# Optimization experiments

Hardware: AMD Instinct MI355X
Metric: run time of the kernel (lower is better)

## Reference

```python
import jax, jax.numpy as jnp
import numpy as np

V, E, F, K, Y = 50000, 128, 256, 3, 1000  # vocab, embed, filters, kernel, labels


def setup_inputs() -> dict:
    key = jax.random.key(0)
    ks = jax.random.split(key, 8)
    x = jax.random.randint(ks[0], (16, 4096), 0, V)
    target = jax.random.randint(ks[1], (16,), 0, Y)
    embed_w = jax.random.normal(ks[2], (V, E), dtype=jnp.float32) * 0.02
    embed_w = embed_w.at[0].set(0.0)  # padding_idx=0
    conv_w = jax.random.normal(ks[3], (F, E, K), dtype=jnp.float32) * (1.0 / np.sqrt(E * K))
    conv_b = jnp.zeros((F,), dtype=jnp.float32)
    U_w = jax.random.normal(ks[4], (Y, F), dtype=jnp.float32) * (1.0 / np.sqrt(F))
    fc_w = jax.random.normal(ks[5], (Y, F), dtype=jnp.float32) * (1.0 / np.sqrt(F))
    fc_b = jnp.zeros((Y,), dtype=jnp.float32)
    return {"x": x, "target": target, "embed_w": embed_w, "conv_w": conv_w,
            "conv_b": conv_b, "U_w": U_w, "fc_w": fc_w, "fc_b": fc_b}


def reference(x, target, embed_w, conv_w, conv_b, U_w, fc_w, fc_b):
    # embedding lookup: (B, L, E); dropout is identity in eval mode
    h = embed_w[x]
    h = jnp.transpose(h, (0, 2, 1))  # (B, E, L)
    # conv1d, SAME padding (pad = floor(K/2) = 1 for K=3)
    h = jax.lax.conv_general_dilated(
        h, conv_w, window_strides=(1,), padding="SAME",
        dimension_numbers=("NCH", "OIH", "NCH"))
    h = jax.nn.relu(h + conv_b[None, :, None])  # (B, F, L)
    # label-wise attention: scores (B, Y, L), softmax over L
    scores = jnp.einsum("yf,bfl->byl", U_w, h)
    alpha = jax.nn.softmax(scores, axis=2)
    # attend: m (B, Y, F)
    m = jnp.einsum("byl,bfl->byf", alpha, h)
    # per-label dot with fc rows + bias -> logits (B, Y)
    logit = jnp.sum(fc_w[None] * m, axis=2) + fc_b
    # cross-entropy loss (target='drg')
    logp = jax.nn.log_softmax(logit, axis=1)
    loss = -jnp.mean(jnp.take_along_axis(logp, target[:, None], axis=1))
    return (logit, loss)
```

## Files before the change

kernel.cpp:

```cpp
#include <hip/hip_runtime.h>
#include <math.h>

using short8   = __attribute__((ext_vector_type(8)))  short;
using floatx4  = __attribute__((ext_vector_type(4)))  float;
using floatx16 = __attribute__((ext_vector_type(16))) float;
using uintx4   = __attribute__((ext_vector_type(4)))  unsigned int;

#define AS1 __attribute__((address_space(1)))
#define AS3 __attribute__((address_space(3)))

__device__ __forceinline__ unsigned short f2bf(float f) {
  union { float f; unsigned int u; } v; v.f = f;
  unsigned int r = v.u + 0x7FFFu + ((v.u >> 16) & 1u);
  return (unsigned short)(r >> 16);
}
__device__ __forceinline__ void gload_lds16(const void* g, void* l) {
  __builtin_amdgcn_global_load_lds((const AS1 unsigned int*)g, (AS3 unsigned int*)l, 16, 0, 0);
}

#define B_  16
#define L_  4096
#define E_  128
#define F_  256
#define Y_  1000

#define OFF_HLF   0u
#define OFF_UBF   33554432u
#define OFF_FBF   34078720u
#define OFF_WBF   34603008u
#define OFF_PART  34799616u
#define OFF_LOSST 35323904u

__global__ __launch_bounds__(256) void k_repack_u(const float* __restrict__ src,
                                                  unsigned short* __restrict__ dst) {
  int i = blockIdx.x * 256 + threadIdx.x;
  int y = i >> 8, f = i & 255;
  float v = (y < Y_) ? src[y * F_ + f] : 0.f;
  dst[i] = f2bf(v);
}

__global__ __launch_bounds__(256) void k_repack_w(const float* __restrict__ cw,
                                                  unsigned short* __restrict__ wbf) {
  int i = blockIdx.x * 256 + threadIdx.x;
  const float* s = cw + (size_t)i * 3;
  wbf[0 * 32768 + i] = f2bf(s[0]);
  wbf[1 * 32768 + i] = f2bf(s[1]);
  wbf[2 * 32768 + i] = f2bf(s[2]);
}

#define ET_STR 272
__global__ __launch_bounds__(256, 4) void k_conv(const unsigned short* __restrict__ wbf,
                                                 const float* __restrict__ conv_b,
                                                 const int* __restrict__ x,
                                                 const float* __restrict__ ew,
                                                 unsigned short* __restrict__ hlf) {
  __shared__ unsigned char et[66 * ET_STR];
  const int tid = threadIdx.x, bid = blockIdx.x;
  const int b = bid >> 6, l0 = (bid & 63) << 6;
  const int w = tid >> 6, lane = tid & 63, c = lane & 15, q = lane >> 4;
  const int* xb = x + b * L_;
  for (int s = tid; s < 1056; s += 256) {
    int row = s >> 4, sg = s & 15;
    int l = l0 - 1 + row;
    int idx = (l >= 0 && l < L_) ? xb[l] : 0;
    const float4* src = (const float4*)(ew + (size_t)idx * E_ + sg * 8);
    float4 a = src[0], bb = src[1];
    uintx4 v;
    v.x = (unsigned int)f2bf(a.x) | ((unsigned int)f2bf(a.y) << 16);
    v.y = (unsigned int)f2bf(a.z) | ((unsigned int)f2bf(a.w) << 16);
    v.z = (unsigned int)f2bf(bb.x) | ((unsigned int)f2bf(bb.y) << 16);
    v.w = (unsigned int)f2bf(bb.z) | ((unsigned int)f2bf(bb.w) << 16);
    *(uintx4*)(et + row * ET_STR + sg * 16) = v;
  }
  __syncthreads();
  const int fw = w * 64;
  floatx4 acc[4][4];
  #pragma unroll
  for (int ms = 0; ms < 4; ++ms)
    #pragma unroll
    for (int nt = 0; nt < 4; ++nt) acc[ms][nt] = (floatx4){0.f, 0.f, 0.f, 0.f};
  #pragma unroll
  for (int d = 0; d < 3; ++d)
    #pragma unroll
    for (int kq = 0; kq < 4; ++kq) {
      short8 aa[4], bb[4];
      #pragma unroll
      for (int ms = 0; ms < 4; ++ms)
        aa[ms] = *(const short8*)(et + (ms * 16 + q * 4 + (0) + c * 0 + 0 + (ms * 0)) * 0 +
                                  (ms * 16 + c + d) * ET_STR + kq * 64 + q * 16);
      #pragma unroll
      for (int nt = 0; nt < 4; ++nt)
        bb[nt] = *(const short8*)((const unsigned char*)wbf +
                   ((size_t)(d * F_ + fw + nt * 16 + c) * E_ + kq * 32 + q * 8) * 2);
      #pragma unroll
      for (int ms = 0; ms < 4; ++ms)
        #pragma unroll
        for (int nt = 0; nt < 4; ++nt)
          acc[ms][nt] = __builtin_amdgcn_mfma_f32_16x16x32_bf16(aa[ms], bb[nt], acc[ms][nt], 0, 0, 0);
    }
  #pragma unroll
  for (int nt = 0; nt < 4; ++nt) {
    int f = fw + nt * 16 + c;
    float bias = conv_b[f];
    #pragma unroll
    for (int ms = 0; ms < 4; ++ms)
      #pragma unroll
      for (int r = 0; r < 4; ++r) {
        int l = l0 + ms * 16 + q * 4 + r;
        float v = acc[ms][nt][r] + bias;
        v = v > 0.f ? v : 0.f;
        hlf[((size_t)b * L_ + l) * F_ + f] = f2bf(v);
      }
  }
}

__global__ __launch_bounds__(256, 2) void k_attn(const unsigned short* __restrict__ ubf,
                                                 const unsigned short* __restrict__ fbf,
                                                 const unsigned short* __restrict__ hlf,
                                                 float2* __restrict__ part) {
  __shared__ unsigned char lds[32768];
  const int tid = threadIdx.x;
  const int w = tid >> 6, lane = tid & 63, lo = lane & 31, hi = lane >> 5;
  const int bid = blockIdx.x;
  const int xcd = bid & 7, r0 = bid >> 3;
  const int b = xcd * 2 + (r0 & 1);
  const int r2 = r0 >> 1, yt = r2 & 7, chunk = r2 >> 3;
  const int y0 = yt << 7, yw = y0 + w * 32;
  short8 uf[16], ff[16];
  #pragma unroll
  for (int ks = 0; ks < 16; ++ks) {
    size_t off = ((size_t)(yw + lo) * F_ + ks * 16 + hi * 8) * 2;
    uf[ks] = *(const short8*)((const unsigned char*)ubf + off);
    ff[ks] = *(const short8*)((const unsigned char*)fbf + off);
  }
  float num[16], den[16];
  #pragma unroll
  for (int r = 0; r < 16; ++r) { num[r] = 0.f; den[r] = 0.f; }
  const unsigned char* hlfb = (const unsigned char*)hlf + (size_t)b * L_ * (F_ * 2);
  const int l0base = chunk << 10;

#define STAGE(dstbuf, l0v)                                                      \
  {                                                                             \
    unsigned char* dstb = (dstbuf);                                             \
    _Pragma("unroll")                                                           \
    for (int ii = 0; ii < 4; ++ii) {                                            \
      int i = w * 4 + ii;                                                       \
      int r = 2 * i + hi;                                                       \
      int g = lo ^ r;                                                           \
      gload_lds16(hlfb + (size_t)((l0v) + r) * 512 + g * 16, dstb + i * 1024);  \
    }                                                                           \
  }

  STAGE(lds, l0base);
  __syncthreads();
  for (int it = 0; it < 32; ++it) {
    unsigned char* cur = lds + ((it & 1) << 14);
    if (it < 31) STAGE(lds + (((it & 1) ^ 1) << 14), l0base + (it + 1) * 32);
    floatx16 S = {0.f,0.f,0.f,0.f,0.f,0.f,0.f,0.f,0.f,0.f,0.f,0.f,0.f,0.f,0.f,0.f};
    floatx16 G = {0.f,0.f,0.f,0.f,0.f,0.f,0.f,0.f,0.f,0.f,0.f,0.f,0.f,0.f,0.f,0.f};
    #pragma unroll
    for (int ks = 0; ks < 16; ++ks) {
      short8 bb = *(const short8*)(cur + lo * 512 + (((ks * 2 + hi) ^ lo) << 4));
      S = __builtin_amdgcn_mfma_f32_32x32x16_bf16(uf[ks], bb, S, 0, 0, 0);
      G = __builtin_amdgcn_mfma_f32_32x32x16_bf16(ff[ks], bb, G, 0, 0, 0);
    }
    #pragma unroll
    for (int r = 0; r < 16; ++r) {
      float p = __expf(S[r]);
      num[r] += p * G[r];
      den[r] += p;
    }
    __syncthreads();
  }
  #pragma unroll
  for (int r = 0; r < 16; ++r) {
    float n = num[r], d = den[r];
    n += __shfl_xor(n, 1, 64);  d += __shfl_xor(d, 1, 64);
    n += __shfl_xor(n, 2, 64);  d += __shfl_xor(d, 2, 64);
    n += __shfl_xor(n, 4, 64);  d += __shfl_xor(d, 4, 64);
    n += __shfl_xor(n, 8, 64);  d += __shfl_xor(d, 8, 64);
    n += __shfl_xor(n, 16, 64); d += __shfl_xor(d, 16, 64);
    num[r] = n; den[r] = d;
  }
  float2* pb = part + (size_t)((b * 8 + yt) * 4 + chunk) * 128;
  if (lo == 0) {
    #pragma unroll
    for (int r = 0; r < 16; ++r) {
      int yl = w * 32 + (r & 3) + 8 * (r >> 2) + 4 * hi;
      float2 v; v.x = num[r]; v.y = den[r];
      pb[yl] = v;
    }
  }
}

__global__ __launch_bounds__(256) void k_logits(const float2* __restrict__ part,
                                                const float* __restrict__ fcb,
                                                const int* __restrict__ target,
                                                float* __restrict__ out,
                                                float* __restrict__ losst) {
  __shared__ float red[4];
  const int b = blockIdx.x, tid = threadIdx.x;
  const int w = tid >> 6;
  float lg[4];
  #pragma unroll
  for (int k = 0; k < 4; ++k) {
    int y = tid + k * 256;
    int yt = y >> 7, yl = y & 127;
    float n = 0.f, la = 0.f;
    #pragma unroll
    for (int ch = 0; ch < 4; ++ch) {
      float2 v = part[(size_t)((b * 8 + yt) * 4 + ch) * 128 + yl];
      n += v.x; la += v.y;
    }
    float lv = (y < Y_) ? (n / la + fcb[y]) : -1e30f;
    lg[k] = lv;
    if (y < Y_) out[b * Y_ + y] = lv;
  }
  float m = fmaxf(fmaxf(lg[0], lg[1]), fmaxf(lg[2], lg[3]));
  for (int off = 1; off < 64; off <<= 1) m = fmaxf(m, __shfl_xor(m, off, 64));
  if ((tid & 63) == 0) red[w] = m;
  __syncthreads();
  m = fmaxf(fmaxf(red[0], red[1]), fmaxf(red[2], red[3]));
  __syncthreads();
  float s = 0.f;
  #pragma unroll
  for (int k = 0; k < 4; ++k)
    if (tid + k * 256 < Y_) s += __expf(lg[k] - m);
  for (int off = 1; off < 64; off <<= 1) s += __shfl_xor(s, off, 64);
  if ((tid & 63) == 0) red[w] = s;
  __syncthreads();
  s = red[0] + red[1] + red[2] + red[3];
  int t = target[b];
  #pragma unroll
  for (int k = 0; k < 4; ++k)
    if (tid + k * 256 == t) losst[b] = -(lg[k] - m - logf(s));
}

__global__ __launch_bounds__(64) void k_sum(const float* __restrict__ losst,
                                            float* __restrict__ out) {
  int lane = threadIdx.x;
  float v = (lane < B_) ? losst[lane] : 0.f;
  v += __shfl_xor(v, 1, 64); v += __shfl_xor(v, 2, 64);
  v += __shfl_xor(v, 4, 64); v += __shfl_xor(v, 8, 64);
  if (lane == 0) out[B_ * Y_] = v * (1.f / (float)B_);
}

extern "C" void kernel_launch(void* const* d_in, const int* in_sizes, int n_in,
                              void* d_out, int out_size, void* d_ws, size_t ws_size,
                              hipStream_t stream) {
  const int*   x       = (const int*)d_in[0];
  const int*   target  = (const int*)d_in[1];
  const float* embed_w = (const float*)d_in[2];
  const float* conv_w  = (const float*)d_in[3];
  const float* conv_b  = (const float*)d_in[4];
  const float* U_w     = (const float*)d_in[5];
  const float* fc_w    = (const float*)d_in[6];
  const float* fc_b    = (const float*)d_in[7];
  float* out = (float*)d_out;
  unsigned char* ws = (unsigned char*)d_ws;
  unsigned short* hlf   = (unsigned short*)(ws + OFF_HLF);
  unsigned short* ubf   = (unsigned short*)(ws + OFF_UBF);
  unsigned short* fbf   = (unsigned short*)(ws + OFF_FBF);
  unsigned short* wbf   = (unsigned short*)(ws + OFF_WBF);
  float2*         part  = (float2*)(ws + OFF_PART);
  float*          losst = (float*)(ws + OFF_LOSST);

  k_repack_u<<<1024, 256, 0, stream>>>(U_w, ubf);
  k_repack_u<<<1024, 256, 0, stream>>>(fc_w, fbf);
  k_repack_w<<<128, 256, 0, stream>>>(conv_w, wbf);
  k_conv<<<1024, 256, 0, stream>>>(wbf, conv_b, x, embed_w, hlf);
  k_attn<<<512, 256, 0, stream>>>(ubf, fbf, hlf, part);
  k_logits<<<16, 256, 0, stream>>>(part, fc_b, target, out, losst);
  k_sum<<<1, 64, 0, stream>>>(losst, out);
}
```

Before: 185.7 us.

## Fuse weight repacks into attention, stage conv output via LDS, merge loss kernels

Removes the two U/fc bf16 repack kernels by having the attention kernel load fp32 weights and convert them in registers, overlapping with the first LDS stage. Conv output is written through LDS and then stored as coalesced 16-byte rows instead of scattered 2-byte stores, at the cost of a larger LDS allocation and lower occupancy hint. The logits and loss-sum kernels are merged into a single 1024-thread block, one wave per batch. These changes cut launch count and improve store coalescing, while adding redundant fp32-to-bf16 conversion work per attention block.

```diff
diff --git a/kernel.cpp b/kernel.cpp
--- a/kernel.cpp
+++ b/kernel.cpp
@@ -25,19 +25,8 @@
 #define Y_  1000
 
 #define OFF_HLF   0u
-#define OFF_UBF   33554432u
-#define OFF_FBF   34078720u
-#define OFF_WBF   34603008u
-#define OFF_PART  34799616u
-#define OFF_LOSST 35323904u
-
-__global__ __launch_bounds__(256) void k_repack_u(const float* __restrict__ src,
-                                                  unsigned short* __restrict__ dst) {
-  int i = blockIdx.x * 256 + threadIdx.x;
-  int y = i >> 8, f = i & 255;
-  float v = (y < Y_) ? src[y * F_ + f] : 0.f;
-  dst[i] = f2bf(v);
-}
+#define OFF_WBF   33554432u
+#define OFF_PART  33751040u
 
 __global__ __launch_bounds__(256) void k_repack_w(const float* __restrict__ cw,
                                                   unsigned short* __restrict__ wbf) {
@@ -49,12 +38,13 @@
 }
 
 #define ET_STR 272
-__global__ __launch_bounds__(256, 4) void k_conv(const unsigned short* __restrict__ wbf,
+__global__ __launch_bounds__(256, 2) void k_conv(const unsigned short* __restrict__ wbf,
                                                  const float* __restrict__ conv_b,
                                                  const int* __restrict__ x,
                                                  const float* __restrict__ ew,
                                                  unsigned short* __restrict__ hlf) {
-  __shared__ unsigned char et[66 * ET_STR];
+  __shared__ unsigned char lds[32768];
+  unsigned char* et = lds;
   const int tid = threadIdx.x, bid = blockIdx.x;
   const int b = bid >> 6, l0 = (bid & 63) << 6;
   const int w = tid >> 6, lane = tid & 63, c = lane & 15, q = lane >> 4;
@@ -86,8 +76,7 @@
       short8 aa[4], bb[4];
       #pragma unroll
       for (int ms = 0; ms < 4; ++ms)
-        aa[ms] = *(const short8*)(et + (ms * 16 + q * 4 + (0) + c * 0 + 0 + (ms * 0)) * 0 +
-                                  (ms * 16 + c + d) * ET_STR + kq * 64 + q * 16);
+        aa[ms] = *(const short8*)(et + (ms * 16 + c + d) * ET_STR + kq * 64 + q * 16);
       #pragma unroll
       for (int nt = 0; nt < 4; ++nt)
         bb[nt] = *(const short8*)((const unsigned char*)wbf +
@@ -98,6 +87,8 @@
         for (int nt = 0; nt < 4; ++nt)
           acc[ms][nt] = __builtin_amdgcn_mfma_f32_16x16x32_bf16(aa[ms], bb[nt], acc[ms][nt], 0, 0, 0);
     }
+  __syncthreads();
+  unsigned char* tl = lds;
   #pragma unroll
   for (int nt = 0; nt < 4; ++nt) {
     int f = fw + nt * 16 + c;
@@ -106,16 +97,21 @@
     for (int ms = 0; ms < 4; ++ms)
       #pragma unroll
       for (int r = 0; r < 4; ++r) {
-        int l = l0 + ms * 16 + q * 4 + r;
         float v = acc[ms][nt][r] + bias;
         v = v > 0.f ? v : 0.f;
-        hlf[((size_t)b * L_ + l) * F_ + f] = f2bf(v);
+        *(unsigned short*)(tl + (ms * 16 + q * 4 + r) * 512 + f * 2) = f2bf(v);
       }
   }
-}
-
-__global__ __launch_bounds__(256, 2) void k_attn(const unsigned short* __restrict__ ubf,
-                                                 const unsigned short* __restrict__ fbf,
+  __syncthreads();
+  unsigned char* hb = (unsigned char*)hlf + ((size_t)b * L_ + l0) * (F_ * 2);
+  for (int s = tid; s < 2048; s += 256) {
+    int row = s >> 5, sg = s & 31;
+    *(uintx4*)(hb + (size_t)row * 512 + sg * 16) = *(const uintx4*)(tl + row * 512 + sg * 16);
+  }
+}
+
+__global__ __launch_bounds__(256, 2) void k_attn(const float* __restrict__ Uw,
+                                                 const float* __restrict__ Fw,
                                                  const unsigned short* __restrict__ hlf,
                                                  float2* __restrict__ part) {
   __shared__ unsigned char lds[32768];
@@ -126,16 +122,6 @@
   const int b = xcd * 2 + (r0 & 1);
   const int r2 = r0 >> 1, yt = r2 & 7, chunk = r2 >> 3;
   const int y0 = yt << 7, yw = y0 + w * 32;
-  short8 uf[16], ff[16];
-  #pragma unroll
-  for (int ks = 0; ks < 16; ++ks) {
-    size_t off = ((size_t)(yw + lo) * F_ + ks * 16 + hi * 8) * 2;
-    uf[ks] = *(const short8*)((const unsigned char*)ubf + off);
-    ff[ks] = *(const short8*)((const unsigned char*)fbf + off);
-  }
-  float num[16], den[16];
-  #pragma unroll
-  for (int r = 0; r < 16; ++r) { num[r] = 0.f; den[r] = 0.f; }
   const unsigned char* hlfb = (const unsigned char*)hlf + (size_t)b * L_ * (F_ * 2);
   const int l0base = chunk << 10;
 
@@ -152,12 +138,32 @@
   }
 
   STAGE(lds, l0base);
+  const int ya = yw + lo;
+  const bool yv = (ya < Y_);
+  const float* up = Uw + (size_t)(yv ? ya : 0) * F_;
+  const float* fp = Fw + (size_t)(yv ? ya : 0) * F_;
+  short8 uf[16], ff[16];
+  #pragma unroll
+  for (int ks = 0; ks < 16; ++ks) {
+    short8 u, f;
+    #pragma unroll
+    for (int j = 0; j < 8; ++j) {
+      float uvv = yv ? up[ks * 16 + hi * 8 + j] : 0.f;
+      float fvv = yv ? fp[ks * 16 + hi * 8 + j] : 0.f;
+      u[j] = (short)f2bf(uvv);
+      f[j] = (short)f2bf(fvv);
+    }
+    uf[ks] = u; ff[ks] = f;
+  }
+  float num[16], den[16];
+  #pragma unroll
+  for (int r = 0; r < 16; ++r) { num[r] = 0.f; den[r] = 0.f; }
   __syncthreads();
   for (int it = 0; it < 32; ++it) {
     unsigned char* cur = lds + ((it & 1) << 14);
     if (it < 31) STAGE(lds + (((it & 1) ^ 1) << 14), l0base + (it + 1) * 32);
     floatx16 S = {0.f,0.f,0.f,0.f,0.f,0.f,0.f,0.f,0.f,0.f,0.f,0.f,0.f,0.f,0.f,0.f};
-    floatx16 G = {0.f,0.f,0.f,0.f,0.f,0.f,0.f,0.f,0.f,0.f,0.f,0.f,0.f,0.f,0.f,0.f};
+    floatx16 G = S;
     #pragma unroll
     for (int ks = 0; ks < 16; ++ks) {
       short8 bb = *(const short8*)(cur + lo * 512 + (((ks * 2 + hi) ^ lo) << 4));
@@ -193,18 +199,18 @@
   }
 }
 
-__global__ __launch_bounds__(256) void k_logits(const float2* __restrict__ part,
-                                                const float* __restrict__ fcb,
-                                                const int* __restrict__ target,
-                                                float* __restrict__ out,
-                                                float* __restrict__ losst) {
-  __shared__ float red[4];
-  const int b = blockIdx.x, tid = threadIdx.x;
-  const int w = tid >> 6;
-  float lg[4];
-  #pragma unroll
-  for (int k = 0; k < 4; ++k) {
-    int y = tid + k * 256;
+__global__ __launch_bounds__(1024) void k_logits(const float2* __restrict__ part,
+                                                 const float* __restrict__ fcb,
+                                                 const int* __restrict__ target,
+                                                 float* __restrict__ out) {
+  __shared__ float wloss[16];
+  const int tid = threadIdx.x, w = tid >> 6, lane = tid & 63;
+  const int b = w, t = target[b];
+  float lg[16];
+  float m = -1e30f;
+  #pragma unroll
+  for (int j = 0; j < 16; ++j) {
+    int y = lane + j * 64;
     int yt = y >> 7, yl = y & 127;
     float n = 0.f, la = 0.f;
     #pragma unroll
@@ -213,36 +219,30 @@
       n += v.x; la += v.y;
     }
     float lv = (y < Y_) ? (n / la + fcb[y]) : -1e30f;
-    lg[k] = lv;
+    lg[j] = lv;
+    m = fmaxf(m, lv);
     if (y < Y_) out[b * Y_ + y] = lv;
   }
-  float m = fmaxf(fmaxf(lg[0], lg[1]), fmaxf(lg[2], lg[3]));
   for (int off = 1; off < 64; off <<= 1) m = fmaxf(m, __shfl_xor(m, off, 64));
-  if ((tid & 63) == 0) red[w] = m;
-  __syncthreads();
-  m = fmaxf(fmaxf(red[0], red[1]), fmaxf(red[2], red[3]));
-  __syncthreads();
-  float s = 0.f;
-  #pragma unroll
-  for (int k = 0; k < 4; ++k)
-    if (tid + k * 256 < Y_) s += __expf(lg[k] - m);
-  for (int off = 1; off < 64; off <<= 1) s += __shfl_xor(s, off, 64);
-  if ((tid & 63) == 0) red[w] = s;
-  __syncthreads();
-  s = red[0] + red[1] + red[2] + red[3];
-  int t = target[b];
-  #pragma unroll
-  for (int k = 0; k < 4; ++k)
-    if (tid + k * 256 == t) losst[b] = -(lg[k] - m - logf(s));
-}
-
-__global__ __launch_bounds__(64) void k_sum(const float* __restrict__ losst,
-                                            float* __restrict__ out) {
-  int lane = threadIdx.x;
-  float v = (lane < B_) ? losst[lane] : 0.f;
-  v += __shfl_xor(v, 1, 64); v += __shfl_xor(v, 2, 64);
-  v += __shfl_xor(v, 4, 64); v += __shfl_xor(v, 8, 64);
-  if (lane == 0) out[B_ * Y_] = v * (1.f / (float)B_);
+  float s = 0.f, lt = 0.f;
+  #pragma unroll
+  for (int j = 0; j < 16; ++j) {
+    int y = lane + j * 64;
+    if (y < Y_) s += __expf(lg[j] - m);
+    if (y == t) lt = lg[j];
+  }
+  for (int off = 1; off < 64; off <<= 1) {
+    s += __shfl_xor(s, off, 64);
+    lt += __shfl_xor(lt, off, 64);
+  }
+  if (lane == 0) wloss[w] = -(lt - m - logf(s));
+  __syncthreads();
+  if (tid == 0) {
+    float acc = 0.f;
+    #pragma unroll
+    for (int i = 0; i < 16; ++i) acc += wloss[i];
+    out[B_ * Y_] = acc * (1.f / (float)B_);
+  }
 }
 
 extern "C" void kernel_launch(void* const* d_in, const int* in_sizes, int n_in,
@@ -258,18 +258,12 @@
   const float* fc_b    = (const float*)d_in[7];
   float* out = (float*)d_out;
   unsigned char* ws = (unsigned char*)d_ws;
-  unsigned short* hlf   = (unsigned short*)(ws + OFF_HLF);
-  unsigned short* ubf   = (unsigned short*)(ws + OFF_UBF);
-  unsigned short* fbf   = (unsigned short*)(ws + OFF_FBF);
-  unsigned short* wbf   = (unsigned short*)(ws + OFF_WBF);
-  float2*         part  = (float2*)(ws + OFF_PART);
-  float*          losst = (float*)(ws + OFF_LOSST);
-
-  k_repack_u<<<1024, 256, 0, stream>>>(U_w, ubf);
-  k_repack_u<<<1024, 256, 0, stream>>>(fc_w, fbf);
+  unsigned short* hlf  = (unsigned short*)(ws + OFF_HLF);
+  unsigned short* wbf  = (unsigned short*)(ws + OFF_WBF);
+  float2*         part = (float2*)(ws + OFF_PART);
+
   k_repack_w<<<128, 256, 0, stream>>>(conv_w, wbf);
   k_conv<<<1024, 256, 0, stream>>>(wbf, conv_b, x, embed_w, hlf);
-  k_attn<<<512, 256, 0, stream>>>(ubf, fbf, hlf, part);
-  k_logits<<<16, 256, 0, stream>>>(part, fc_b, target, out, losst);
-  k_sum<<<1, 64, 0, stream>>>(losst, out);
-}
+  k_attn<<<512, 256, 0, stream>>>(U_w, fc_w, hlf, part);
+  k_logits<<<1, 1024, 0, stream>>>(part, fc_b, target, out);
+}
```

Result: slower. 243.8 us (+31.3%).
